# Kernel optimization log

Measured on AMD Instinct MI355X. Metric: run time of the kernel, lower is better.

## Reference

```python
import jax, jax.numpy as jnp
import numpy as np

OVERSAMP = 2.0
D = 2  # spatial dims


def _pad_center(x, grid):
    # centered zero-pad of last D dims from im_size to grid (PadLast)
    H, W = x.shape[-2], x.shape[-1]
    ph, pw = grid[0] - H, grid[1] - W
    pads = [(0, 0)] * (x.ndim - 2) + [(ph // 2, ph - ph // 2), (pw // 2, pw - pw // 2)]
    return jnp.pad(x, pads)


def _crop_center(x, im_size):
    # adjoint of centered pad: crop last D dims back to im_size
    H2, W2 = x.shape[-2], x.shape[-1]
    ph, pw = H2 - im_size[0], W2 - im_size[1]
    return x[..., ph // 2: ph // 2 + im_size[0], pw // 2: pw // 2 + im_size[1]]


def setup_inputs() -> dict:
    key = jax.random.key(0)
    ks = jax.random.split(key, 6)
    N, A, C, H, W = 2, 5, 12, 256, 256
    G = (2 * H, 2 * W)  # oversampled grid for toeplitz kernels
    return {
        "x_r": jax.random.normal(ks[0], (N, A, H, W), jnp.float32),
        "x_i": jax.random.normal(ks[1], (N, A, H, W), jnp.float32),
        "mps_r": jax.random.normal(ks[2], (C, H, W), jnp.float32) * 0.3,
        "mps_i": jax.random.normal(ks[3], (C, H, W), jnp.float32) * 0.3,
        "kernels_r": jax.random.normal(ks[4], (A, A) + G, jnp.float32) * 0.1,
        "kernels_i": jax.random.normal(ks[5], (A, A) + G, jnp.float32) * 0.1,
    }


def reference(x_r, x_i, mps_r, mps_i, kernels_r, kernels_i):
    # Toeplitz normal operator AHA_func from SubspaceLinopFactory.get_normal_toeplitz,
    # fully vectorized over coils (C) and subspace coefficients (A).
    x = x_r + 1j * x_i                    # [N, A, H, W]
    mps = mps_r + 1j * mps_i              # [C, H, W]
    kernels = kernels_r + 1j * kernels_i  # [A_out, A_in, 2H, 2W]
    im_size = x.shape[-2:]
    grid = kernels.shape[-2:]
    axes = (-2, -1)

    # x.unsqueeze(coildim) * mps[:, None]  -> [N, C, A, H, W]
    xm = x[:, None, :, :, :] * mps[None, :, None, :, :]
    # PadLast: centered zero-pad to the oversampled grid
    xp = _pad_center(xm, grid)                             # [N, C, A, 2H, 2W]
    Fx = jnp.fft.fftn(xp, axes=axes, norm="ortho")         # [N, C, A_in, 2H, 2W]
    # Fx.unsqueeze(2) * kernels[A_out, A_in], summed over A_in
    G = jnp.einsum("ncahw,bahw->ncbhw", Fx, kernels)       # [N, C, A_out, 2H, 2W]
    y = (OVERSAMP ** D) * jnp.fft.ifftn(G, axes=axes, norm="ortho")
    yc = _crop_center(y, im_size)                          # [N, C, A_out, H, W]
    # multiply conj coil maps, sum over coils
    out = jnp.einsum("ncahw,chw->nahw", yc, jnp.conj(mps))  # [N, A, H, W] complex64
    return out
```

## Files before the change

### kernel.cpp

```cpp
#include <hip/hip_runtime.h>
#include <math.h>

#define N_ 2
#define A_ 5
#define C_ 12
#define H_ 256
#define G_ 512
#define SCALE_ (4.0f / 262144.0f)
#define OUTF_ 655360
#define HALFF_ 327680
#define IMGC_ 131072

struct __attribute__((aligned(4))) h2 { _Float16 x, y; };
struct __attribute__((aligned(8))) h2x2 { _Float16 x0, y0, x1, y1; };
__device__ __forceinline__ float2 ld2(const h2* p, size_t i) {
    h2 v = p[i]; return make_float2((float)v.x, (float)v.y);
}
__device__ __forceinline__ void st2(h2* p, size_t i, float2 v) {
    float x = fminf(fmaxf(v.x, -60000.f), 60000.f);
    float y = fminf(fmaxf(v.y, -60000.f), 60000.f);
    h2 o; o.x = (_Float16)x; o.y = (_Float16)y; p[i] = o;
}

__device__ __forceinline__ float2 cmul(float2 a, float2 b) {
    return make_float2(a.x * b.x - a.y * b.y, a.x * b.y + a.y * b.x);
}

__device__ __forceinline__ float4 qadd(float4 a, float4 b) {
    return make_float4(a.x + b.x, a.y + b.y, a.z + b.z, a.w + b.w);
}
__device__ __forceinline__ float4 qsub(float4 a, float4 b) {
    return make_float4(a.x - b.x, a.y - b.y, a.z - b.z, a.w - b.w);
}
__device__ __forceinline__ float4 qmul(float4 a, float4 w) {
    return make_float4(a.x * w.x - a.y * w.y, a.x * w.y + a.y * w.x,
                       a.z * w.z - a.w * w.w, a.z * w.w + a.w * w.z);
}
__device__ __forceinline__ float4 qmulc(float4 a, float4 w) {
    return make_float4(a.x * w.x + a.y * w.y, a.y * w.x - a.x * w.y,
                       a.z * w.z + a.w * w.w, a.w * w.z - a.z * w.w);
}
__device__ __forceinline__ int PHI(int i) { return i ^ ((i >> 3) & 7); }

__device__ __forceinline__ void build_twS(float2* twS, int t) {
    if (t < 256) {
        float s, c;
        sincosf(-6.283185307179586f * (float)t * (1.0f / 512.0f), &s, &c);
        twS[t] = make_float2(c, s);
    }
    __syncthreads();
    int off = 256;
    #pragma unroll
    for (int sh = 1; sh <= 8; sh++) {
        int sz = 256 >> sh;
        if (t < sz) twS[off + t] = twS[t << sh];
        off += sz;
    }
    __syncthreads();
}

__device__ __forceinline__ void fwd_quad(float4* D, const float4* tw4,
                                         int bt, int M4, int offA4) {
    int jf = bt & (M4 - 1);
    int f0 = ((bt & ~(M4 - 1)) << 2) | jf;
    float4 x0 = D[PHI(f0)],          x1 = D[PHI(f0 + M4)];
    float4 x2 = D[PHI(f0 + 2 * M4)], x3 = D[PHI(f0 + 3 * M4)];
    float4 tA  = tw4[offA4 + jf];
    float4 tA2 = tw4[offA4 + M4 + jf];
    float4 tB  = tw4[offA4 + 2 * M4 + jf];
    float4 u0 = qadd(x0, x2), v0 = qmul(qsub(x0, x2), tA);
    float4 u1 = qadd(x1, x3), v1 = qmul(qsub(x1, x3), tA2);
    D[PHI(f0)]          = qadd(u0, u1);
    D[PHI(f0 + M4)]     = qmul(qsub(u0, u1), tB);
    D[PHI(f0 + 2 * M4)] = qadd(v0, v1);
    D[PHI(f0 + 3 * M4)] = qmul(qsub(v0, v1), tB);
}
__device__ __forceinline__ void inv_quad(float4* D, const float4* tw4,
                                         int bt, int M2, int offM4, int off2M4) {
    int jf = bt & (M2 - 1);
    int f0 = ((bt & ~(M2 - 1)) << 2) | jf;
    float4 x0 = D[PHI(f0)],          x1 = D[PHI(f0 + M2)];
    float4 x2 = D[PHI(f0 + 2 * M2)], x3 = D[PHI(f0 + 3 * M2)];
    float4 wA  = tw4[offM4 + jf];
    float4 wB0 = tw4[off2M4 + jf];
    float4 wB1 = tw4[off2M4 + M2 + jf];
    float4 t1 = qmulc(x1, wA), t3 = qmulc(x3, wA);
    float4 u0 = qadd(x0, t1), u1 = qsub(x0, t1);
    float4 u2 = qadd(x2, t3), u3 = qsub(x2, t3);
    float4 s2 = qmulc(u2, wB0), s3 = qmulc(u3, wB1);
    D[PHI(f0)]          = qadd(u0, s2);
    D[PHI(f0 + M2)]     = qadd(u1, s3);
    D[PHI(f0 + 2 * M2)] = qsub(u0, s2);
    D[PHI(f0 + 3 * M2)] = qsub(u1, s3);
}

__device__ void fft512_dif(float2* d, const float2* twS, int t) {
    int off = 0;
    #pragma unroll
    for (int m = 256; m >= 1; m >>= 1) {
        if (m >= 64) __syncthreads();
        else __builtin_amdgcn_wave_barrier();
        int j = t & (m - 1);
        int p = ((t & ~(m - 1)) << 1) | j;
        int q = p + m;
        float2 a = d[p], b = d[q];
        d[p] = make_float2(a.x + b.x, a.y + b.y);
        float2 s = make_float2(a.x - b.x, a.y - b.y);
        d[q] = cmul(s, twS[off + j]);
        off += m;
    }
    __syncthreads();
}
__device__ void ifft512_dit(float2* d, const float2* twS, int t) {
    int off = 510;
    #pragma unroll
    for (int m = 1; m <= 256; m <<= 1) {
        if (m == 1 || m >= 128) __syncthreads();
        else __builtin_amdgcn_wave_barrier();
        int j = t & (m - 1);
        int p = ((t & ~(m - 1)) << 1) | j;
        int q = p + m;
        float2 w = twS[off + j];
        w.y = -w.y;
        float2 b = cmul(d[q], w);
        float2 a = d[p];
        d[p] = make_float2(a.x + b.x, a.y + b.y);
        d[q] = make_float2(a.x - b.x, a.y - b.y);
        off -= (m << 1);
    }
    __syncthreads();
}

__global__ __launch_bounds__(256)
void zeroF(float* outf, int base) {
    outf[(size_t)base + blockIdx.x * 256 + threadIdx.x] = 0.f;
}


__global__ __launch_bounds__(256)
void kernelR(const float* __restrict__ kr, const float* __restrict__ ki,
             h2* Krev) {
    int p = blockIdx.x >> 9;
    int h = blockIdx.x & 511;
    int t = threadIdx.x;
    size_t base = ((size_t)p * G_ + h) * G_;
    int j0 = __brev((unsigned)t) >> 23;
    int j1 = __brev((unsigned)(t + 256)) >> 23;
    st2(Krev, base + t,       make_float2(kr[base + j0], ki[base + j0]));
    st2(Krev, base + t + 256, make_float2(kr[base + j1], ki[base + j1]));
}

__global__ __launch_bounds__(256)
void kernelA2(const float* __restrict__ xr, const float* __restrict__ xi,
              const float* __restrict__ mr, const float* __restrict__ mi,
              h2* P, int n0, int nspan) {
    int blk = blockIdx.x;
    int oct = blk & 31;
    int a   = (blk >> 5) % 5;
    int rest = blk / 160;
    int c  = rest % 12;
    int nl = rest / 12;
    int n  = n0 + nl;
    int t = threadIdx.x;
    __shared__ float2 twS[512];
    __shared__ float4 rows4[8][262];
    build_twS(twS, t);
    const float4* tw4 = (const float4*)twS;

    int r = t & 7;
    int wc = oct * 8 + r;
    float2* rowf2 = (float2*)&rows4[r][0];
    #pragma unroll
    for (int k = 0; k < 8; k++) {
        int h = (t >> 3) + 32 * k;
        size_t xo = (((size_t)n * A_ + a) * H_ + h) * H_ + wc;
        size_t mo = (((size_t)c) * H_ + h) * H_ + wc;
        float xr_ = xr[xo], xi_ = xi[xo];
        float mr_ = mr[mo], mi_ = mi[mo];
        int e = h + 128;
        rowf2[2 * PHI(e >> 1) + (e & 1)] =
            make_float2(xr_ * mr_ - xi_ * mi_, xr_ * mi_ + xi_ * mr_);
        int z = (h < 128) ? h : (h + 256);
        rowf2[2 * PHI(z >> 1) + (z & 1)] = make_float2(0.f, 0.f);
    }
    __syncthreads();

    int wv = t >> 6, ln = t & 63;
    float4* d0 = &rows4[2 * wv][0];
    float4* d1 = &rows4[2 * wv + 1][0];
    fwd_quad(d0, tw4, ln, 64, 0);   fwd_quad(d1, tw4, ln, 64, 0);
    __builtin_amdgcn_wave_barrier();
    fwd_quad(d0, tw4, ln, 16, 192); fwd_quad(d1, tw4, ln, 16, 192);
    __builtin_amdgcn_wave_barrier();
    fwd_quad(d0, tw4, ln, 4, 240);  fwd_quad(d1, tw4, ln, 4, 240);
    __builtin_amdgcn_wave_barrier();
    fwd_quad(d0, tw4, ln, 1, 252);  fwd_quad(d1, tw4, ln, 1, 252);
    __syncthreads();

    h2* Pp = P + (size_t)((nl * 12 + c) * 5 + a) * IMGC_;
    #pragma unroll
    for (int k = 0; k < 16; k++) {
        int jh = k * 32 + (t >> 3);
        float4 v = rows4[r][PHI(jh >> 1)];
        float2 res = (jh & 1) ? make_float2(v.x - v.z, v.y - v.w)
                              : make_float2(v.x + v.z, v.y + v.w);
        st2(Pp, (size_t)jh * 256 + oct * 8 + r, res);
    }
}

__global__ __launch_bounds__(320)
void kernelB2(const h2* __restrict__ Krev, h2* P, int nspan) {
    int blk = blockIdx.x;
    int xcd = blk & 7;
    int idx = blk >> 3;
    int cn  = 12 * nspan;
    int jh  = xcd * 64 + idx / cn;
    int rem = idx % cn;
    int c   = rem % 12;
    int nl  = rem / 12;
    int htrue = __brev((unsigned)jh) >> 23;
    int t = threadIdx.x;
    __shared__ float2 twS[512];
    __shared__ float4 Fa4[5][256];
    build_twS(twS, t);
    const float4* tw4 = (const float4*)twS;
    int wv = t >> 6, ln = t & 63;
    size_t pbase = (size_t)((nl * 12 + c) * 5) * IMGC_ + (size_t)jh * 256;

    float2* Ff2 = (float2*)&Fa4[wv][0];
    const h2* Pa = P + pbase + (size_t)wv * IMGC_;
    #pragma unroll
    for (int k = 0; k < 4; k++) {
        int e = ln + 64 * k;
        float2 v = ld2(Pa, e);
        int ec = e + 128;
        Ff2[2 * PHI(ec >> 1) + (ec & 1)] = v;
        int z = (e < 128) ? e : (e + 256);
        Ff2[2 * PHI(z >> 1) + (z & 1)] = make_float2(0.f, 0.f);
    }
    __builtin_amdgcn_wave_barrier();

    float4* D = &Fa4[wv][0];
    fwd_quad(D, tw4, ln, 64, 0);   __builtin_amdgcn_wave_barrier();
    fwd_quad(D, tw4, ln, 16, 192); __builtin_amdgcn_wave_barrier();
    fwd_quad(D, tw4, ln, 4, 240);  __builtin_amdgcn_wave_barrier();
    fwd_quad(D, tw4, ln, 1, 252);
    __syncthreads();

    if (t < 256) {
        float2 f0[5], f1[5];
        #pragma unroll
        for (int a = 0; a < 5; a++) {
            float4 x = Fa4[a][PHI(t)];
            f0[a] = make_float2(x.x + x.z, x.y + x.w);
            f1[a] = make_float2(x.x - x.z, x.y - x.w);
        }
        const h2x2* Kp = reinterpret_cast<const h2x2*>(Krev);
        #pragma unroll
        for (int b = 0; b < 5; b++) {
            float2 a0 = make_float2(0.f, 0.f);
            float2 a1 = make_float2(0.f, 0.f);
            #pragma unroll
            for (int a = 0; a < 5; a++) {
                h2x2 kv = Kp[((size_t)(b * 5 + a) * G_ + htrue) * 256 + t];
                float k0x = (float)kv.x0, k0y = (float)kv.y0;
                float k1x = (float)kv.x1, k1y = (float)kv.y1;
                a0.x += k0x * f0[a].x - k0y * f0[a].y;
                a0.y += k0x * f0[a].y + k0y * f0[a].x;
                a1.x += k1x * f1[a].x - k1y * f1[a].y;
                a1.y += k1x * f1[a].y + k1y * f1[a].x;
            }
            Fa4[b][PHI(t)] =
                make_float4(a0.x + a1.x, a0.y + a1.y, a0.x - a1.x, a0.y - a1.y);
        }
    }
    __syncthreads();

    inv_quad(D, tw4, ln, 1, 254, 252);  __builtin_amdgcn_wave_barrier();
    inv_quad(D, tw4, ln, 4, 248, 240);  __builtin_amdgcn_wave_barrier();
    inv_quad(D, tw4, ln, 16, 224, 192); __builtin_amdgcn_wave_barrier();
    inv_quad(D, tw4, ln, 64, 128, 0);
    __builtin_amdgcn_wave_barrier();

    h2* Pb = P + pbase + (size_t)wv * IMGC_;
    #pragma unroll
    for (int k = 0; k < 4; k++) {
        int e = ln + 64 * k;
        int ec = e + 128;
        float2 v = Ff2[2 * PHI(ec >> 1) + (ec & 1)];
        st2(Pb, e, v);
    }
}

__global__ __launch_bounds__(256)
void kernelC2(const float* __restrict__ mr, const float* __restrict__ mi,
              const h2* __restrict__ P, float* outf, int n0, int nspan) {
    int blk = blockIdx.x;
    int oct = blk & 31;
    int b   = (blk >> 5) % 5;
    int rest = blk / 160;
    int c  = rest % 12;
    int nl = rest / 12;
    int n  = n0 + nl;
    int t = threadIdx.x;
    __shared__ float2 twS[512];
    __shared__ float4 rows4[8][262];
    build_twS(twS, t);
    const float4* tw4 = (const float4*)twS;

    int r = t & 7;
    int wc = oct * 8 + r;
    const h2* Pb = P + (size_t)((nl * 12 + c) * 5 + b) * IMGC_;
    #pragma unroll
    for (int k = 0; k < 8; k++) {
        int jh0 = k * 64 + (t >> 3) * 2;
        float2 p0 = ld2(Pb, (size_t)jh0 * 256 + wc);
        float2 p1 = ld2(Pb, (size_t)(jh0 + 1) * 256 + wc);
        rows4[r][PHI(jh0 >> 1)] =
            make_float4(p0.x + p1.x, p0.y + p1.y, p0.x - p1.x, p0.y - p1.y);
    }
    __syncthreads();

    int wv = t >> 6, ln = t & 63;
    float4* d0 = &rows4[2 * wv][0];
    float4* d1 = &rows4[2 * wv + 1][0];
    inv_quad(d0, tw4, ln, 1, 254, 252);  inv_quad(d1, tw4, ln, 1, 254, 252);
    __builtin_amdgcn_wave_barrier();
    inv_quad(d0, tw4, ln, 4, 248, 240);  inv_quad(d1, tw4, ln, 4, 248, 240);
    __builtin_amdgcn_wave_barrier();
    inv_quad(d0, tw4, ln, 16, 224, 192); inv_quad(d1, tw4, ln, 16, 224, 192);
    __builtin_amdgcn_wave_barrier();
    inv_quad(d0, tw4, ln, 64, 128, 0);   inv_quad(d1, tw4, ln, 64, 128, 0);
    __syncthreads();

    const float2* rowf2 = (const float2*)&rows4[r][0];
    #pragma unroll
    for (int k = 0; k < 8; k++) {
        int hh = (t >> 3) + 32 * k;
        int e = hh + 128;
        float2 v = rowf2[2 * PHI(e >> 1) + (e & 1)];
        size_t mo = (((size_t)c) * H_ + hh) * H_ + wc;
        float m_r = mr[mo], m_i = mi[mo];
        float re = (m_r * v.x + m_i * v.y) * SCALE_;
        size_t idx = (((size_t)n * A_ + b) * H_ + hh) * H_ + wc;
        unsafeAtomicAdd(&outf[idx], re);
    }
}


__global__ __launch_bounds__(256)
void kernelA(const float* __restrict__ xr, const float* __restrict__ xi,
             const float* __restrict__ mr, const float* __restrict__ mi,
             h2* X1, int n, int c, int a) {
    int oct = blockIdx.x;
    int t = threadIdx.x;
    __shared__ float2 twS[512];
    __shared__ float2 rows[8][516];
    build_twS(twS, t);

    int r = t & 7;
    int wc = oct * 8 + r;
    #pragma unroll
    for (int k = 0; k < 8; k++) {
        int h = (t >> 3) + 32 * k;
        size_t xo = (((size_t)n * A_ + a) * H_ + h) * H_ + wc;
        size_t mo = (((size_t)c) * H_ + h) * H_ + wc;
        float xr_ = xr[xo], xi_ = xi[xo];
        float mr_ = mr[mo], mi_ = mi[mo];
        rows[r][h + 128] = make_float2(xr_ * mr_ - xi_ * mi_,
                                       xr_ * mi_ + xi_ * mr_);
        rows[r][(h < 128) ? h : (h + 256)] = make_float2(0.f, 0.f);
    }
    __syncthreads();
    for (int rr = 0; rr < 8; rr++) fft512_dif(&rows[rr][0], twS, t);

    #pragma unroll
    for (int k = 0; k < 16; k++) {
        int jh = k * 32 + (t >> 3);
        st2(X1, (size_t)jh * 256 + oct * 8 + (t & 7), rows[t & 7][jh]);
    }
}

__global__ __launch_bounds__(256)
void kernelB(const float* __restrict__ kr, const float* __restrict__ ki,
             const h2* X1, h2* X2, int b, int a) {
    int jh = blockIdx.x;
    int htrue = __brev((unsigned)jh) >> 23;
    int t = threadIdx.x;
    __shared__ float2 twS[512];
    __shared__ float2 F[512];
    __shared__ float2 g[512];
    build_twS(twS, t);

    float2 v = ld2(X1, (size_t)jh * 256 + t);
    F[t + 128] = v;
    F[(t < 128) ? t : (t + 256)] = make_float2(0.f, 0.f);
    __syncthreads();
    fft512_dif(F, twS, t);

    #pragma unroll
    for (int half = 0; half < 2; half++) {
        int jw = t + half * 256;
        int wtrue = __brev((unsigned)jw) >> 23;
        size_t kidx = (((size_t)(b * A_ + a)) * G_ + htrue) * G_ + wtrue;
        g[jw] = cmul(make_float2(kr[kidx], ki[kidx]), F[jw]);
    }
    ifft512_dit(g, twS, t);

    float2 res = g[t + 128];
    size_t o = (size_t)jh * 256 + t;
    if (a == 0) st2(X2, o, res);
    else {
        float2 cur = ld2(X2, o);
        st2(X2, o, make_float2(cur.x + res.x, cur.y + res.y));
    }
}

__global__ __launch_bounds__(256)
void kernelC(const float* __restrict__ mr, const float* __restrict__ mi,
             const h2* X2, float* outf, int n, int c, int b) {
    int oct = blockIdx.x;
    int t = threadIdx.x;
    __shared__ float2 twS[512];
    __shared__ float2 rows[8][516];
    build_twS(twS, t);

    #pragma unroll
    for (int k = 0; k < 16; k++) {
        int jh = k * 32 + (t >> 3);
        rows[t & 7][jh] = ld2(X2, (size_t)jh * 256 + oct * 8 + (t & 7));
    }
    for (int rr = 0; rr < 8; rr++) ifft512_dit(&rows[rr][0], twS, t);

    int r = t & 7;
    int wc = oct * 8 + r;
    #pragma unroll
    for (int k = 0; k < 8; k++) {
        int hh = (t >> 3) + 32 * k;
        float2 v = rows[r][hh + 128];
        size_t mo = (((size_t)c) * H_ + hh) * H_ + wc;
        float m_r = mr[mo], m_i = mi[mo];
        float re = (m_r * v.x + m_i * v.y) * SCALE_;
        size_t idx = (((size_t)n * A_ + b) * H_ + hh) * H_ + wc;
        outf[idx] += re;
    }
}

extern "C" void kernel_launch(void* const* d_in, const int* in_sizes, int n_in,
                              void* d_out, int out_size, void* d_ws, size_t ws_size,
                              hipStream_t stream) {
    const float* xr = (const float*)d_in[0];
    const float* xi = (const float*)d_in[1];
    const float* mr = (const float*)d_in[2];
    const float* mi = (const float*)d_in[3];
    const float* kr = (const float*)d_in[4];
    const float* ki = (const float*)d_in[5];
    float* outf = (float*)d_out;
    (void)in_sizes; (void)n_in; (void)out_size;

    const size_t KREV_BYTES = 25ull * G_ * G_ * sizeof(h2);
    const size_t PLANES1    = 60ull * IMGC_ * sizeof(h2);
    const size_t PLANES2    = 120ull * IMGC_ * sizeof(h2);

    if (d_ws != nullptr && ws_size >= PLANES2 + KREV_BYTES) {
        h2* P    = (h2*)d_ws;
        h2* Krev = (h2*)((char*)d_ws + PLANES2);
        zeroF<<<OUTF_ / 256, 256, 0, stream>>>(outf, 0);
        kernelR<<<25 * 512, 256, 0, stream>>>(kr, ki, Krev);
        kernelA2<<<2 * C_ * A_ * 32, 256, 0, stream>>>(xr, xi, mr, mi, P, 0, 2);
        kernelB2<<<2 * C_ * 512, 320, 0, stream>>>(Krev, P, 2);
        kernelC2<<<2 * C_ * A_ * 32, 256, 0, stream>>>(mr, mi, P, outf, 0, 2);
        return;
    }

    if (d_ws != nullptr && ws_size >= PLANES1 + KREV_BYTES) {
        h2* P    = (h2*)d_ws;
        h2* Krev = (h2*)((char*)d_ws + PLANES1);
        zeroF<<<OUTF_ / 256, 256, 0, stream>>>(outf, 0);
        kernelR<<<25 * 512, 256, 0, stream>>>(kr, ki, Krev);
        for (int n = 0; n < N_; n++) {
            kernelA2<<<C_ * A_ * 32, 256, 0, stream>>>(xr, xi, mr, mi, P, n, 1);
            kernelB2<<<C_ * 512, 320, 0, stream>>>(Krev, P, 1);
            kernelC2<<<C_ * A_ * 32, 256, 0, stream>>>(mr, mi, P, outf, n, 1);
        }
        return;
    }

    zeroF<<<HALFF_ / 256, 256, 0, stream>>>(outf, 0);
    {
        h2* X1 = (h2*)(outf + HALFF_);
        h2* X2 = (h2*)(outf + HALFF_ + IMGC_);
        for (int c = 0; c < C_; c++)
            for (int b = 0; b < A_; b++) {
                for (int a = 0; a < A_; a++) {
                    kernelA<<<32, 256, 0, stream>>>(xr, xi, mr, mi, X1, 0, c, a);
                    kernelB<<<512, 256, 0, stream>>>(kr, ki, X1, X2, b, a);
                }
                kernelC<<<32, 256, 0, stream>>>(mr, mi, X2, outf, 0, c, b);
            }
    }

    zeroF<<<HALFF_ / 256, 256, 0, stream>>>(outf, HALFF_);
    {
        h2* X1 = (h2*)d_in[0];
        h2* X2 = (h2*)d_in[1];
        for (int c = 0; c < C_; c++)
            for (int b = 0; b < A_; b++) {
                for (int a = 0; a < A_; a++) {
                    kernelA<<<32, 256, 0, stream>>>(xr, xi, mr, mi, X1, 1, c, a);
                    kernelB<<<512, 256, 0, stream>>>(kr, ki, X1, X2, b, a);
                }
                kernelC<<<32, 256, 0, stream>>>(mr, mi, X2, outf, 1, c, b);
            }
    }
}
```

Before: 382.0 us.

## Loop subspace coefficients in forward FFT and group coils in inverse FFT kernel

The forward column-FFT kernel now handles all five subspace coefficients per block in a loop, so each coil-map tile is loaded into registers once and reused. The inverse kernel processes three coils per block and accumulates their coil-combined results in registers before a single atomic add, which cuts global atomics to a third. In exchange there are fewer blocks (768 and 1280 instead of 3840), so occupancy and latency hiding drop, and the per-block loops add extra barriers.

```diff
diff --git a/kernel.cpp b/kernel.cpp
--- a/kernel.cpp
+++ b/kernel.cpp
@@ -10,6 +10,7 @@
 #define OUTF_ 655360
 #define HALFF_ 327680
 #define IMGC_ 131072
+#define NCG_ 4
 
 struct __attribute__((aligned(4))) h2 { _Float16 x, y; };
 struct __attribute__((aligned(8))) h2x2 { _Float16 x0, y0, x1, y1; };
@@ -156,8 +157,7 @@
               h2* P, int n0, int nspan) {
     int blk = blockIdx.x;
     int oct = blk & 31;
-    int a   = (blk >> 5) % 5;
-    int rest = blk / 160;
+    int rest = blk >> 5;
     int c  = rest % 12;
     int nl = rest / 12;
     int n  = n0 + nl;
@@ -169,42 +169,52 @@
 
     int r = t & 7;
     int wc = oct * 8 + r;
-    float2* rowf2 = (float2*)&rows4[r][0];
+    float mR[8], mI[8];
     #pragma unroll
     for (int k = 0; k < 8; k++) {
         int h = (t >> 3) + 32 * k;
-        size_t xo = (((size_t)n * A_ + a) * H_ + h) * H_ + wc;
-        size_t mo = (((size_t)c) * H_ + h) * H_ + wc;
-        float xr_ = xr[xo], xi_ = xi[xo];
-        float mr_ = mr[mo], mi_ = mi[mo];
-        int e = h + 128;
-        rowf2[2 * PHI(e >> 1) + (e & 1)] =
-            make_float2(xr_ * mr_ - xi_ * mi_, xr_ * mi_ + xi_ * mr_);
-        int z = (h < 128) ? h : (h + 256);
-        rowf2[2 * PHI(z >> 1) + (z & 1)] = make_float2(0.f, 0.f);
-    }
-    __syncthreads();
-
+        size_t mo = ((size_t)c * H_ + h) * H_ + wc;
+        mR[k] = mr[mo]; mI[k] = mi[mo];
+    }
+    float2* rowf2 = (float2*)&rows4[r][0];
     int wv = t >> 6, ln = t & 63;
     float4* d0 = &rows4[2 * wv][0];
     float4* d1 = &rows4[2 * wv + 1][0];
-    fwd_quad(d0, tw4, ln, 64, 0);   fwd_quad(d1, tw4, ln, 64, 0);
-    __builtin_amdgcn_wave_barrier();
-    fwd_quad(d0, tw4, ln, 16, 192); fwd_quad(d1, tw4, ln, 16, 192);
-    __builtin_amdgcn_wave_barrier();
-    fwd_quad(d0, tw4, ln, 4, 240);  fwd_quad(d1, tw4, ln, 4, 240);
-    __builtin_amdgcn_wave_barrier();
-    fwd_quad(d0, tw4, ln, 1, 252);  fwd_quad(d1, tw4, ln, 1, 252);
-    __syncthreads();
-
-    h2* Pp = P + (size_t)((nl * 12 + c) * 5 + a) * IMGC_;
-    #pragma unroll
-    for (int k = 0; k < 16; k++) {
-        int jh = k * 32 + (t >> 3);
-        float4 v = rows4[r][PHI(jh >> 1)];
-        float2 res = (jh & 1) ? make_float2(v.x - v.z, v.y - v.w)
-                              : make_float2(v.x + v.z, v.y + v.w);
-        st2(Pp, (size_t)jh * 256 + oct * 8 + r, res);
+
+    for (int a = 0; a < 5; a++) {
+        #pragma unroll
+        for (int k = 0; k < 8; k++) {
+            int h = (t >> 3) + 32 * k;
+            size_t xo = (((size_t)n * A_ + a) * H_ + h) * H_ + wc;
+            float xr_ = xr[xo], xi_ = xi[xo];
+            int e = h + 128;
+            rowf2[2 * PHI(e >> 1) + (e & 1)] =
+                make_float2(xr_ * mR[k] - xi_ * mI[k],
+                            xr_ * mI[k] + xi_ * mR[k]);
+            int z = (h < 128) ? h : (h + 256);
+            rowf2[2 * PHI(z >> 1) + (z & 1)] = make_float2(0.f, 0.f);
+        }
+        __syncthreads();
+
+        fwd_quad(d0, tw4, ln, 64, 0);   fwd_quad(d1, tw4, ln, 64, 0);
+        __builtin_amdgcn_wave_barrier();
+        fwd_quad(d0, tw4, ln, 16, 192); fwd_quad(d1, tw4, ln, 16, 192);
+        __builtin_amdgcn_wave_barrier();
+        fwd_quad(d0, tw4, ln, 4, 240);  fwd_quad(d1, tw4, ln, 4, 240);
+        __builtin_amdgcn_wave_barrier();
+        fwd_quad(d0, tw4, ln, 1, 252);  fwd_quad(d1, tw4, ln, 1, 252);
+        __syncthreads();
+
+        h2* Pp = P + (size_t)((nl * 12 + c) * 5 + a) * IMGC_;
+        #pragma unroll
+        for (int k = 0; k < 16; k++) {
+            int jh = k * 32 + (t >> 3);
+            float4 v = rows4[r][PHI(jh >> 1)];
+            float2 res = (jh & 1) ? make_float2(v.x - v.z, v.y - v.w)
+                                  : make_float2(v.x + v.z, v.y + v.w);
+            st2(Pp, (size_t)jh * 256 + oct * 8 + r, res);
+        }
+        __syncthreads();
     }
 }
 
@@ -299,8 +309,8 @@
     int oct = blk & 31;
     int b   = (blk >> 5) % 5;
     int rest = blk / 160;
-    int c  = rest % 12;
-    int nl = rest / 12;
+    int cg = rest % NCG_;
+    int nl = rest / NCG_;
     int n  = n0 + nl;
     int t = threadIdx.x;
     __shared__ float2 twS[512];
@@ -310,40 +320,53 @@
 
     int r = t & 7;
     int wc = oct * 8 + r;
-    const h2* Pb = P + (size_t)((nl * 12 + c) * 5 + b) * IMGC_;
-    #pragma unroll
-    for (int k = 0; k < 8; k++) {
-        int jh0 = k * 64 + (t >> 3) * 2;
-        float2 p0 = ld2(Pb, (size_t)jh0 * 256 + wc);
-        float2 p1 = ld2(Pb, (size_t)(jh0 + 1) * 256 + wc);
-        rows4[r][PHI(jh0 >> 1)] =
-            make_float4(p0.x + p1.x, p0.y + p1.y, p0.x - p1.x, p0.y - p1.y);
-    }
-    __syncthreads();
-
     int wv = t >> 6, ln = t & 63;
     float4* d0 = &rows4[2 * wv][0];
     float4* d1 = &rows4[2 * wv + 1][0];
-    inv_quad(d0, tw4, ln, 1, 254, 252);  inv_quad(d1, tw4, ln, 1, 254, 252);
-    __builtin_amdgcn_wave_barrier();
-    inv_quad(d0, tw4, ln, 4, 248, 240);  inv_quad(d1, tw4, ln, 4, 248, 240);
-    __builtin_amdgcn_wave_barrier();
-    inv_quad(d0, tw4, ln, 16, 224, 192); inv_quad(d1, tw4, ln, 16, 224, 192);
-    __builtin_amdgcn_wave_barrier();
-    inv_quad(d0, tw4, ln, 64, 128, 0);   inv_quad(d1, tw4, ln, 64, 128, 0);
-    __syncthreads();
-
     const float2* rowf2 = (const float2*)&rows4[r][0];
+
+    float acc[8];
+    #pragma unroll
+    for (int k = 0; k < 8; k++) acc[k] = 0.f;
+
+    for (int ci = 0; ci < 3; ci++) {
+        int c = cg * 3 + ci;
+        const h2* Pb = P + (size_t)((nl * 12 + c) * 5 + b) * IMGC_;
+        #pragma unroll
+        for (int k = 0; k < 8; k++) {
+            int jh0 = k * 64 + (t >> 3) * 2;
+            float2 p0 = ld2(Pb, (size_t)jh0 * 256 + wc);
+            float2 p1 = ld2(Pb, (size_t)(jh0 + 1) * 256 + wc);
+            rows4[r][PHI(jh0 >> 1)] =
+                make_float4(p0.x + p1.x, p0.y + p1.y, p0.x - p1.x, p0.y - p1.y);
+        }
+        __syncthreads();
+
+        inv_quad(d0, tw4, ln, 1, 254, 252);  inv_quad(d1, tw4, ln, 1, 254, 252);
+        __builtin_amdgcn_wave_barrier();
+        inv_quad(d0, tw4, ln, 4, 248, 240);  inv_quad(d1, tw4, ln, 4, 248, 240);
+        __builtin_amdgcn_wave_barrier();
+        inv_quad(d0, tw4, ln, 16, 224, 192); inv_quad(d1, tw4, ln, 16, 224, 192);
+        __builtin_amdgcn_wave_barrier();
+        inv_quad(d0, tw4, ln, 64, 128, 0);   inv_quad(d1, tw4, ln, 64, 128, 0);
+        __syncthreads();
+
+        #pragma unroll
+        for (int k = 0; k < 8; k++) {
+            int hh = (t >> 3) + 32 * k;
+            int e = hh + 128;
+            float2 v = rowf2[2 * PHI(e >> 1) + (e & 1)];
+            size_t mo = (((size_t)c) * H_ + hh) * H_ + wc;
+            acc[k] += mr[mo] * v.x + mi[mo] * v.y;
+        }
+        __syncthreads();
+    }
+
     #pragma unroll
     for (int k = 0; k < 8; k++) {
         int hh = (t >> 3) + 32 * k;
-        int e = hh + 128;
-        float2 v = rowf2[2 * PHI(e >> 1) + (e & 1)];
-        size_t mo = (((size_t)c) * H_ + hh) * H_ + wc;
-        float m_r = mr[mo], m_i = mi[mo];
-        float re = (m_r * v.x + m_i * v.y) * SCALE_;
         size_t idx = (((size_t)n * A_ + b) * H_ + hh) * H_ + wc;
-        unsafeAtomicAdd(&outf[idx], re);
+        unsafeAtomicAdd(&outf[idx], acc[k] * SCALE_);
     }
 }
 
@@ -467,9 +490,9 @@
         h2* Krev = (h2*)((char*)d_ws + PLANES2);
         zeroF<<<OUTF_ / 256, 256, 0, stream>>>(outf, 0);
         kernelR<<<25 * 512, 256, 0, stream>>>(kr, ki, Krev);
-        kernelA2<<<2 * C_ * A_ * 32, 256, 0, stream>>>(xr, xi, mr, mi, P, 0, 2);
+        kernelA2<<<2 * C_ * 32, 256, 0, stream>>>(xr, xi, mr, mi, P, 0, 2);
         kernelB2<<<2 * C_ * 512, 320, 0, stream>>>(Krev, P, 2);
-        kernelC2<<<2 * C_ * A_ * 32, 256, 0, stream>>>(mr, mi, P, outf, 0, 2);
+        kernelC2<<<2 * A_ * 32 * NCG_, 256, 0, stream>>>(mr, mi, P, outf, 0, 2);
         return;
     }
 
@@ -479,9 +502,9 @@
         zeroF<<<OUTF_ / 256, 256, 0, stream>>>(outf, 0);
         kernelR<<<25 * 512, 256, 0, stream>>>(kr, ki, Krev);
         for (int n = 0; n < N_; n++) {
-            kernelA2<<<C_ * A_ * 32, 256, 0, stream>>>(xr, xi, mr, mi, P, n, 1);
+            kernelA2<<<C_ * 32, 256, 0, stream>>>(xr, xi, mr, mi, P, n, 1);
             kernelB2<<<C_ * 512, 320, 0, stream>>>(Krev, P, 1);
-            kernelC2<<<C_ * A_ * 32, 256, 0, stream>>>(mr, mi, P, outf, n, 1);
+            kernelC2<<<A_ * 32 * NCG_, 256, 0, stream>>>(mr, mi, P, outf, n, 1);
         }
         return;
     }
```

Measured after the change: 386.9 us. About the same (+1.3%).
